# Optimization experiments

Hardware: AMD Instinct MI355X
Metric: run time of the kernel (lower is better)

## Reference

```python
import jax, jax.numpy as jnp
import numpy as np

BS, NF, N, J, NOUT = 8, 64, 2048, 3, 64
EPS = 1e-5


def setup_inputs() -> dict:
    key = jax.random.key(0)
    ks = jax.random.split(key, 6)
    X = jax.random.normal(ks[0], (BS, NF, N), dtype=jnp.float32)
    W = jax.random.normal(ks[1], (BS, N, N, J), dtype=jnp.float32)
    N_batch = jnp.ones((BS,), jnp.float32) * N  # valid nodes per graph
    mask = jnp.ones((BS, 1, N), jnp.float32)
    scale = 0.1  # matches _init_weights
    cv1_w = scale * jax.random.normal(ks[2], (NOUT, J * NF), jnp.float32)
    cv1_b = scale * jax.random.normal(ks[3], (NOUT,), jnp.float32)
    cv2_w = scale * jax.random.normal(ks[4], (NOUT, J * NF), jnp.float32)
    cv2_b = scale * jax.random.normal(ks[5], (NOUT,), jnp.float32)
    bn_gamma = jnp.ones((2 * NOUT,), jnp.float32)
    bn_beta = jnp.zeros((2 * NOUT,), jnp.float32)
    return {"X": X, "W": W, "N_batch": N_batch, "mask": mask,
            "cv1_w": cv1_w, "cv1_b": cv1_b, "cv2_w": cv2_w, "cv2_b": cv2_b,
            "bn_gamma": bn_gamma, "bn_beta": bn_beta}


def reference(X, W, N_batch, mask, cv1_w, cv1_b, cv2_w, cv2_b, bn_gamma, bn_beta):
    bs, nf, n = X.shape
    j = W.shape[3]
    # graph_oper: out[b, j*nf:(j+1)*nf, m] = (A[b,:,:,j] @ X[b].T).T
    #           = sum_n W[b,m,n,j] * X[b,f,n]  -> fused batched contraction
    x1 = jnp.einsum('bmnj,bfn->bjfm', W, X).reshape(bs, j * nf, n)
    # conv1x1 (kernel size 1) == per-node matmul over channels
    y1 = jnp.einsum('oi,bin->bon', cv1_w, x1) + cv1_b[None, :, None]
    z1 = jax.nn.relu(y1)
    yl1 = jax.nn.relu(jnp.einsum('oi,bin->bon', cv2_w, x1) + cv2_b[None, :, None])
    zb = jnp.concatenate([yl1, z1], axis=1)  # (bs, 2*NOUT, N)
    # masked graph batch-norm: per-channel stats over all valid nodes in the batch
    total = jnp.sum(N_batch)
    mean = jnp.sum(zb * mask, axis=(0, 2)) / total
    cz = zb - mean[None, :, None]
    var = jnp.sum(mask * cz * cz, axis=(0, 2)) / total
    zbn = cz * jax.lax.rsqrt(var + EPS)[None, :, None]
    zbn = (bn_gamma[None, :, None] * zbn + bn_beta[None, :, None]) * mask
    return (zbn, W)
```

## Files before the change

kernel.cpp:

```cpp
#include <hip/hip_runtime.h>
#include <hip/hip_bf16.h>


#define EPSV 1e-5f
#define ZBN_ELEMS (8*128*2048)

typedef __bf16 bf16x8 __attribute__((ext_vector_type(8)));
typedef float  f32x4  __attribute__((ext_vector_type(4)));
typedef float  f4v    __attribute__((ext_vector_type(4)));

union BF8 { unsigned short u[8]; bf16x8 v; };
union F4  { float f[4]; f4v v; };

__device__ __forceinline__ unsigned short f2bf(float f) {
    unsigned u = __float_as_uint(f);
    u += 0x7fffu + ((u >> 16) & 1u);
    return (unsigned short)(u >> 16);
}

__global__ void prep_kernel(const float* __restrict__ X,
                            unsigned short* __restrict__ Xbf,
                            float* __restrict__ stats) {
    int t = blockIdx.x * 256 + threadIdx.x;
    Xbf[t] = f2bf(X[t]);
    if (blockIdx.x == 0 && threadIdx.x < 256) stats[threadIdx.x] = 0.0f;
}

__global__ __launch_bounds__(256, 4) void gemm_conv_kernel(
    const float* __restrict__ W,
    const unsigned short* __restrict__ Xbf,
    const float* __restrict__ cv1_w, const float* __restrict__ cv1_b,
    const float* __restrict__ cv2_w, const float* __restrict__ cv2_b,
    float* __restrict__ out, float* __restrict__ stats)
{
    __shared__ unsigned short wt[3][16][136];
    __shared__ unsigned short x1s[16][200];

    const int tid  = threadIdx.x;
    const int w    = tid >> 6;
    const int lane = tid & 63;
    const int q    = lane >> 4;
    const int l15  = lane & 15;
    const int b    = blockIdx.x >> 7;
    const int mt   = blockIdx.x & 127;

    const float* Wbase  = W   + (size_t)(b * 2048 + mt * 16) * 6144;
    float*       Wobase = out + (size_t)ZBN_ELEMS + (size_t)(b * 2048 + mt * 16) * 6144;
    const unsigned short* Xrow = Xbf + (size_t)b * (64 * 2048) + (w * 16 + l15) * 2048;

    int gofs[6];
    int crow[6], co4[6];
    #pragma unroll
    for (int i = 0; i < 6; ++i) {
        int c  = tid + 256 * i;
        int r  = c / 96;
        int o4 = (c - r * 96) * 4;
        crow[i] = r; co4[i] = o4;
        gofs[i] = r * 6144 + o4;
    }

    f32x4 acc[3];
    acc[0] = (f32x4)0.0f; acc[1] = (f32x4)0.0f; acc[2] = (f32x4)0.0f;

    auto process = [&](F4 (&buf)[6], int t) {
        #pragma unroll
        for (int i = 0; i < 6; ++i)
            *(f4v*)(Wobase + t * 384 + gofs[i]) = buf[i].v;
        #pragma unroll
        for (int i = 0; i < 6; ++i) {
            #pragma unroll
            for (int u = 0; u < 4; ++u) {
                int o = co4[i] + u;
                int n = o / 3;
                int j = o - n * 3;
                ((unsigned short*)wt)[(j * 16 + crow[i]) * 136 + n] = f2bf(buf[i].f[u]);
            }
        }
        __syncthreads();
        BF8 bfr[4];
        #pragma unroll
        for (int kk = 0; kk < 4; ++kk)
            bfr[kk].v = *(const bf16x8*)(Xrow + t * 128 + kk * 32 + q * 8);
        #pragma unroll
        for (int kk = 0; kk < 4; ++kk) {
            #pragma unroll
            for (int j = 0; j < 3; ++j) {
                bf16x8 af = *(const bf16x8*)&wt[j][l15][kk * 32 + q * 8];
                acc[j] = __builtin_amdgcn_mfma_f32_16x16x32_bf16(af, bfr[kk].v, acc[j], 0, 0, 0);
            }
        }
        __syncthreads();
    };

    F4 bufA[6], bufB[6];
    #pragma unroll
    for (int i = 0; i < 6; ++i)
        bufA[i].v = __builtin_nontemporal_load((const f4v*)(Wbase + gofs[i]));

    #pragma unroll 1
    for (int tt = 0; tt < 8; ++tt) {
        const int t0 = 2 * tt, t1 = 2 * tt + 1;
        #pragma unroll
        for (int i = 0; i < 6; ++i)
            bufB[i].v = __builtin_nontemporal_load((const f4v*)(Wbase + t1 * 384 + gofs[i]));
        process(bufA, t0);
        if (tt < 7) {
            #pragma unroll
            for (int i = 0; i < 6; ++i)
                bufA[i].v = __builtin_nontemporal_load((const f4v*)(Wbase + (t1 + 1) * 384 + gofs[i]));
        }
        process(bufB, t1);
    }

    #pragma unroll
    for (int j = 0; j < 3; ++j)
        #pragma unroll
        for (int r = 0; r < 4; ++r)
            x1s[q * 4 + r][j * 64 + w * 16 + l15] = f2bf(acc[j][r]);
    __syncthreads();

    f32x4 acc2[2];
    acc2[0] = (f32x4)0.0f;
    acc2[1] = (f32x4)0.0f;

    #pragma unroll
    for (int kt = 0; kt < 6; ++kt) {
        const int i0 = kt * 32 + q * 8;
        BF8 afr[2];
        #pragma unroll
        for (int ctl = 0; ctl < 2; ++ctl) {
            const int c = (2 * w + ctl) * 16 + l15;
            const float* wr = (c < 64) ? (cv2_w + c * 192) : (cv1_w + (c - 64) * 192);
            const f4v* wp2 = (const f4v*)(wr + i0);
            f4v w0 = wp2[0], w1 = wp2[1];
            #pragma unroll
            for (int e = 0; e < 4; ++e) {
                afr[ctl].u[e]     = f2bf(w0[e]);
                afr[ctl].u[e + 4] = f2bf(w1[e]);
            }
        }
        BF8 b2;
        b2.v = *(const bf16x8*)(&x1s[l15][i0]);
        #pragma unroll
        for (int ctl = 0; ctl < 2; ++ctl)
            acc2[ctl] = __builtin_amdgcn_mfma_f32_16x16x32_bf16(afr[ctl].v, b2.v, acc2[ctl], 0, 0, 0);
    }

    #pragma unroll
    for (int ctl = 0; ctl < 2; ++ctl) {
        #pragma unroll
        for (int r = 0; r < 4; ++r) {
            const int c = (2 * w + ctl) * 16 + q * 4 + r;
            const float bias = (c < 64) ? cv2_b[c] : cv1_b[c - 64];
            float zv = acc2[ctl][r] + bias;
            zv = fmaxf(zv, 0.0f);
            out[((size_t)(b * 128 + c) << 11) + mt * 16 + l15] = zv;
            float s1 = zv, s2 = zv * zv;
            #pragma unroll
            for (int msk = 1; msk < 16; msk <<= 1) {
                s1 += __shfl_xor(s1, msk);
                s2 += __shfl_xor(s2, msk);
            }
            if (l15 == 0) {
                atomicAdd(&stats[c], s1);
                atomicAdd(&stats[128 + c], s2);
            }
        }
    }
}

__global__ void finalize_kernel(const float* __restrict__ stats,
                                const float* __restrict__ Nb,
                                const float* __restrict__ gamma,
                                const float* __restrict__ beta,
                                float* __restrict__ ss) {
    int c = threadIdx.x;
    float total = 0.0f;
    #pragma unroll
    for (int i = 0; i < 8; ++i) total += Nb[i];
    float mean = stats[c] / total;
    float var  = stats[128 + c] / total - mean * mean;
    float inv  = rsqrtf(var + EPSV);
    float sc   = gamma[c] * inv;
    ss[c]       = sc;
    ss[128 + c] = beta[c] - mean * sc;
}

__global__ void norm_kernel(float* __restrict__ out,
                            const float* __restrict__ ss,
                            const float* __restrict__ mask) {
    int t = blockIdx.x * 256 + threadIdx.x;
    float4 v = ((const float4*)out)[t];
    int row = t >> 9;
    int c = row & 127;
    int b = row >> 7;
    float sc = ss[c], sh = ss[128 + c];
    float4 mk = ((const float4*)mask)[(b << 9) + (t & 511)];
    float4 r;
    r.x = (v.x * sc + sh) * mk.x;
    r.y = (v.y * sc + sh) * mk.y;
    r.z = (v.z * sc + sh) * mk.z;
    r.w = (v.w * sc + sh) * mk.w;
    ((float4*)out)[t] = r;
}

extern "C" void kernel_launch(void* const* d_in, const int* in_sizes, int n_in,
                              void* d_out, int out_size, void* d_ws, size_t ws_size,
                              hipStream_t stream) {
    const float* X     = (const float*)d_in[0];
    const float* W     = (const float*)d_in[1];
    const float* Nb    = (const float*)d_in[2];
    const float* mask  = (const float*)d_in[3];
    const float* cv1_w = (const float*)d_in[4];
    const float* cv1_b = (const float*)d_in[5];
    const float* cv2_w = (const float*)d_in[6];
    const float* cv2_b = (const float*)d_in[7];
    const float* gamma = (const float*)d_in[8];
    const float* beta  = (const float*)d_in[9];
    float* out = (float*)d_out;

    unsigned short* Xbf = (unsigned short*)d_ws;
    float* stats = (float*)((char*)d_ws + (size_t)2 * 1024 * 1024);
    float* ss    = stats + 256;

    hipLaunchKernelGGL(prep_kernel,      dim3(4096), dim3(256), 0, stream, X, Xbf, stats);
    hipLaunchKernelGGL(gemm_conv_kernel, dim3(1024), dim3(256), 0, stream,
                       W, Xbf, cv1_w, cv1_b, cv2_w, cv2_b, out, stats);
    hipLaunchKernelGGL(finalize_kernel,  dim3(1),    dim3(128), 0, stream, stats, Nb, gamma, beta, ss);
    hipLaunchKernelGGL(norm_kernel,      dim3(2048), dim3(256), 0, stream, out, ss, mask);
}
```

Baseline: 771.5 us.

## Double-buffer LDS W tile to drop one barrier per k-step

Each k-step now writes into one of two alternating LDS buffers, so the trailing __syncthreads after the MFMA phase is removed and only a single raw s_barrier remains per step. The X fragment loads and the next W tile prefetch are issued at the start of each step, before the global writes and LDS conversion, to overlap with them. A final __syncthreads is added before x1s is used. The cost is twice the LDS for the W tile, which may reduce occupancy. It also relies on the alternating buffers plus a single barrier being enough to prevent the next-but-one write from overlapping reads still in progress.

```diff
diff --git a/kernel.cpp b/kernel.cpp
--- a/kernel.cpp
+++ b/kernel.cpp
@@ -33,7 +33,7 @@
     const float* __restrict__ cv2_w, const float* __restrict__ cv2_b,
     float* __restrict__ out, float* __restrict__ stats)
 {
-    __shared__ unsigned short wt[3][16][136];
+    __shared__ unsigned short wt[2][3][16][136];
     __shared__ unsigned short x1s[16][200];
 
     const int tid  = threadIdx.x;
@@ -62,10 +62,19 @@
     f32x4 acc[3];
     acc[0] = (f32x4)0.0f; acc[1] = (f32x4)0.0f; acc[2] = (f32x4)0.0f;
 
-    auto process = [&](F4 (&buf)[6], int t) {
+    auto step = [&](F4 (&cur)[6], F4 (&nxt)[6], int t, int lb) {
+        BF8 xr[4];
+        #pragma unroll
+        for (int kk = 0; kk < 4; ++kk)
+            xr[kk].v = *(const bf16x8*)(Xrow + t * 128 + kk * 32 + q * 8);
+        if (t < 15) {
+            #pragma unroll
+            for (int i = 0; i < 6; ++i)
+                nxt[i].v = __builtin_nontemporal_load((const f4v*)(Wbase + (t + 1) * 384 + gofs[i]));
+        }
         #pragma unroll
         for (int i = 0; i < 6; ++i)
-            *(f4v*)(Wobase + t * 384 + gofs[i]) = buf[i].v;
+            *(f4v*)(Wobase + t * 384 + gofs[i]) = cur[i].v;
         #pragma unroll
         for (int i = 0; i < 6; ++i) {
             #pragma unroll
@@ -73,23 +82,20 @@
                 int o = co4[i] + u;
                 int n = o / 3;
                 int j = o - n * 3;
-                ((unsigned short*)wt)[(j * 16 + crow[i]) * 136 + n] = f2bf(buf[i].f[u]);
-            }
-        }
-        __syncthreads();
-        BF8 bfr[4];
-        #pragma unroll
-        for (int kk = 0; kk < 4; ++kk)
-            bfr[kk].v = *(const bf16x8*)(Xrow + t * 128 + kk * 32 + q * 8);
+                ((unsigned short*)wt[lb])[(j * 16 + crow[i]) * 136 + n] = f2bf(cur[i].f[u]);
+            }
+        }
+        asm volatile("s_waitcnt lgkmcnt(0)" ::: "memory");
+        __builtin_amdgcn_s_barrier();
+        __builtin_amdgcn_sched_barrier(0);
         #pragma unroll
         for (int kk = 0; kk < 4; ++kk) {
             #pragma unroll
             for (int j = 0; j < 3; ++j) {
-                bf16x8 af = *(const bf16x8*)&wt[j][l15][kk * 32 + q * 8];
-                acc[j] = __builtin_amdgcn_mfma_f32_16x16x32_bf16(af, bfr[kk].v, acc[j], 0, 0, 0);
-            }
-        }
-        __syncthreads();
+                bf16x8 af = *(const bf16x8*)&wt[lb][j][l15][kk * 32 + q * 8];
+                acc[j] = __builtin_amdgcn_mfma_f32_16x16x32_bf16(af, xr[kk].v, acc[j], 0, 0, 0);
+            }
+        }
     };
 
     F4 bufA[6], bufB[6];
@@ -99,18 +105,11 @@
 
     #pragma unroll 1
     for (int tt = 0; tt < 8; ++tt) {
-        const int t0 = 2 * tt, t1 = 2 * tt + 1;
-        #pragma unroll
-        for (int i = 0; i < 6; ++i)
-            bufB[i].v = __builtin_nontemporal_load((const f4v*)(Wbase + t1 * 384 + gofs[i]));
-        process(bufA, t0);
-        if (tt < 7) {
-            #pragma unroll
-            for (int i = 0; i < 6; ++i)
-                bufA[i].v = __builtin_nontemporal_load((const f4v*)(Wbase + (t1 + 1) * 384 + gofs[i]));
-        }
-        process(bufB, t1);
-    }
+        step(bufA, bufB, 2 * tt,     0);
+        step(bufB, bufA, 2 * tt + 1, 1);
+    }
+
+    __syncthreads();
 
     #pragma unroll
     for (int j = 0; j < 3; ++j)
```

Result: no change. 776.8 us (+0.7%).
